# Performance work log

Measured on AMD Instinct MI355X. Metric: run time of the kernel, lower is better.

Reference implementation:

```python
import jax, jax.numpy as jnp
import numpy as np

TEMPERATURE = 0.5


def setup_inputs() -> dict:
    key = jax.random.key(0)
    k1, k2 = jax.random.split(key)
    B, C, H, W = 64, 256, 32, 32
    inputs = jax.random.normal(k1, (B, C, H, W), dtype=jnp.float32)
    targets = jax.random.normal(k2, (B, C, H, W), dtype=jnp.float32)
    return {"inputs": inputs, "targets": targets}


def reference(inputs, targets):
    # [B, C, H, W] -> [H, W, B, C]
    x = jnp.transpose(inputs, (2, 3, 0, 1))
    y = jnp.transpose(targets, (2, 3, 0, 1))
    B = x.shape[-2]
    feats = jnp.concatenate([x, y], axis=-2)  # [H, W, 2B, C]
    eps = jnp.finfo(feats.dtype).eps
    # cosine similarity: normalize each vector with eps-clamped norm, then dot
    norms = jnp.maximum(jnp.linalg.norm(feats, axis=-1, keepdims=True), eps)
    fn = feats / norms
    sim = jnp.einsum('hwic,hwjc->hwij', fn, fn)  # [H, W, 2B, 2B]
    # mask self-similarity diagonal with -inf
    mask = jnp.eye(2 * B, dtype=bool)
    sim = jnp.where(mask, -jnp.inf, sim)
    log_sm = jax.nn.log_softmax(sim / TEMPERATURE, axis=-1)
    pos = jnp.concatenate(
        [jnp.diagonal(log_sm, offset=B, axis1=-2, axis2=-1),
         jnp.diagonal(log_sm, offset=-B, axis1=-2, axis2=-1)],
        axis=-1,
    )  # [H, W, 2B]
    return -jnp.mean(pos)
```

## Files before the change

kernel.cpp:

```cpp
#include <hip/hip_runtime.h>
#include <stdint.h>

#define HWPOS 1024
#define CCH   256
#define RROWS 128
#define EPSF  1.1920928955078125e-07f

typedef __attribute__((ext_vector_type(4))) float float4v;

__device__ __forceinline__ uint32_t pk4_fp8(float a, float b, float c, float d) {
  int v = 0;
  v = __builtin_amdgcn_cvt_pk_fp8_f32(a, b, v, false);
  v = __builtin_amdgcn_cvt_pk_fp8_f32(c, d, v, true);
  return (uint32_t)v;
}


__global__ __launch_bounds__(256, 4) void k_transpose(const float* __restrict__ inp,
                                                      const float* __restrict__ tgt,
                                                      unsigned char* __restrict__ wsF,
                                                      float* __restrict__ out) {
  const int t    = threadIdx.x;
  const int hq   = t & 7;
  const int dd   = (t >> 3) & 15;
  const int rsel = t >> 7;
  const int r    = blockIdx.y * 2 + rsel;
  const int hw0  = blockIdx.x * 32;
  if (blockIdx.x == 0 && blockIdx.y == 0 && t == 0) out[0] = 0.0f;
  const int m = r & 15;
  const int s = dd ^ m;
  const float* src = (r < 64) ? (inp + (size_t)r * CCH * HWPOS)
                              : (tgt + (size_t)(r - 64) * CCH * HWPOS);
  const float* p = src + (size_t)(dd * 16) * HWPOS + hw0 + hq * 4;
  float4 v[16];
#pragma unroll
  for (int e = 0; e < 16; ++e) v[e] = *(const float4*)(p + (size_t)e * HWPOS);
#pragma unroll
  for (int q = 0; q < 4; ++q) {
    float x[16];
#pragma unroll
    for (int e = 0; e < 16; ++e)
      x[e] = (q == 0) ? v[e].x : (q == 1) ? v[e].y : (q == 2) ? v[e].z : v[e].w;
    uint4 o;
    o.x = pk4_fp8(x[0],  x[1],  x[2],  x[3]);
    o.y = pk4_fp8(x[4],  x[5],  x[6],  x[7]);
    o.z = pk4_fp8(x[8],  x[9],  x[10], x[11]);
    o.w = pk4_fp8(x[12], x[13], x[14], x[15]);
    const size_t a = (size_t)(hw0 + hq * 4 + q) * 32768 + (size_t)r * 256 + s * 16;
    *(uint4*)(wsF + a) = o;
  }
}

__global__ __launch_bounds__(512, 4) void k_gram(const unsigned char* __restrict__ wsF,
                                                 float* __restrict__ out) {
  __shared__ unsigned char Fs[32768];
  __shared__ float sInv[RROWS];
  __shared__ float wred[8];
  const int t  = threadIdx.x;
  const int hw = blockIdx.x;
  const int lane = t & 63;
  const int w    = t >> 6;
  const int lid  = lane & 15;
  const int quad = lane >> 4;
  float4v acc[8];
#pragma unroll
  for (int ni = 0; ni < 8; ++ni) acc[ni] = (float4v){0.f, 0.f, 0.f, 0.f};
  const unsigned char* gsrc = wsF + (size_t)hw * 32768;
#pragma unroll
  for (int it = 0; it < 4; ++it) {
    const size_t ch = (size_t)it * 512 + t;
    __builtin_amdgcn_global_load_lds(
        (const __attribute__((address_space(1))) unsigned int*)(gsrc + ch * 16),
        (__attribute__((address_space(3))) unsigned int*)(Fs + ch * 16),
        16, 0, 0);
  }
  __syncthreads();
  const int rowA = (w << 4) | lid;
#pragma unroll
  for (int ks = 0; ks < 8; ++ks) {
    const int d    = 2 * ks + (quad >> 1);
    const int off  = ((d ^ lid) << 4) + (quad & 1) * 8;
    long a = *(const long*)&Fs[rowA * 256 + off];
#pragma unroll
    for (int ni = 0; ni < 8; ++ni) {
      long b = *(const long*)&Fs[(((ni << 4) | lid)) * 256 + off];
      acc[ni] = __builtin_amdgcn_mfma_f32_16x16x32_fp8_fp8(a, b, acc[ni], 0, 0, 0);
    }
  }
  {
    float diagv = 0.f;
#pragma unroll
    for (int ni = 0; ni < 8; ++ni) {
      if (ni == w) {
#pragma unroll
        for (int e = 0; e < 4; ++e)
          if (e == (lid & 3)) diagv = acc[ni][e];
      }
    }
    if ((lid >> 2) == quad) {
      sInv[(w << 4) | lid] = 1.0f / fmaxf(sqrtf(diagv), EPSF);
    }
  }
  __syncthreads();
  float invj[8];
#pragma unroll
  for (int ni = 0; ni < 8; ++ni) invj[ni] = sInv[(ni << 4) | lid];
  const int tj = (w + 4) & 7;
  float lacc = 0.f;
#pragma unroll
  for (int reg = 0; reg < 4; ++reg) {
    const int rloc = quad * 4 + reg;
    const int rg   = (w << 4) | rloc;
    const float invi = sInv[rg];
    float v[8];
#pragma unroll
    for (int ni = 0; ni < 8; ++ni) v[ni] = 2.0f * acc[ni][reg] * invi * invj[ni];
#pragma unroll
    for (int ni = 0; ni < 8; ++ni)
      if (ni == w && lid == rloc) v[ni] = -3.0e38f;
    float mx = v[0];
#pragma unroll
    for (int ni = 1; ni < 8; ++ni) mx = fmaxf(mx, v[ni]);
#pragma unroll
    for (int sh = 1; sh < 16; sh <<= 1) mx = fmaxf(mx, __shfl_xor(mx, sh, 16));
    float sm = 0.f;
#pragma unroll
    for (int ni = 0; ni < 8; ++ni) sm += __expf(v[ni] - mx);
#pragma unroll
    for (int sh = 1; sh < 16; sh <<= 1) sm += __shfl_xor(sm, sh, 16);
    const float lse = mx + __logf(sm);
    float cand = 0.f;
#pragma unroll
    for (int ni = 0; ni < 8; ++ni)
      if (ni == tj) cand = v[ni];
    const float vp = __shfl(cand, rloc, 16);
    lacc += vp - lse;
  }
#pragma unroll
  for (int sh = 1; sh < 64; sh <<= 1) lacc += __shfl_xor(lacc, sh, 64);
  if (lane == 0) wred[w] = lacc;
  __syncthreads();
  if (t == 0) {
    float tot = 0.f;
#pragma unroll
    for (int i = 0; i < 8; ++i) tot += wred[i];
    atomicAdd(out, -tot * (1.0f / 2097152.0f));
  }
}

extern "C" void kernel_launch(void* const* d_in, const int* in_sizes, int n_in,
                              void* d_out, int out_size, void* d_ws, size_t ws_size,
                              hipStream_t stream) {
  const float* inp = (const float*)d_in[0];
  const float* tgt = (const float*)d_in[1];
  unsigned char* wsF = (unsigned char*)d_ws;
  k_transpose<<<dim3(32, 64), 256, 0, stream>>>(inp, tgt, wsF, (float*)d_out);
  k_gram<<<dim3(HWPOS), 512, 0, stream>>>(wsF, (float*)d_out);
}
```

Measured before the change: 174.6 us.

## Stage fp8 transpose through LDS to coalesce workspace writes

The transpose kernel now packs fp8 values into a swizzled shared-memory tile and then writes 128-byte contiguous runs per row to the workspace. Previously each thread stored isolated 16-byte chunks scattered at a 32 KB stride. The block/grid mapping changes to cover 128 hw positions and half of the channels per block, and the XOR swizzle layout expected by the gram kernel is preserved. This adds a barrier and LDS traffic in exchange for better write coalescing.

```diff
diff --git a/kernel.cpp b/kernel.cpp
--- a/kernel.cpp
+++ b/kernel.cpp
@@ -20,21 +20,22 @@
                                                       const float* __restrict__ tgt,
                                                       unsigned char* __restrict__ wsF,
                                                       float* __restrict__ out) {
+  __shared__ uint4 Ls[1024];
   const int t    = threadIdx.x;
-  const int hq   = t & 7;
-  const int dd   = (t >> 3) & 15;
-  const int rsel = t >> 7;
-  const int r    = blockIdx.y * 2 + rsel;
-  const int hw0  = blockIdx.x * 32;
-  if (blockIdx.x == 0 && blockIdx.y == 0 && t == 0) out[0] = 0.0f;
-  const int m = r & 15;
-  const int s = dd ^ m;
+  const int hq   = t & 31;
+  const int ddl  = t >> 5;
+  const int bx   = blockIdx.x;
+  const int r    = blockIdx.y;
+  const int half = blockIdx.z;
+  if (bx == 0 && r == 0 && half == 0 && t == 0) out[0] = 0.0f;
+  const int dd = half * 8 + ddl;
   const float* src = (r < 64) ? (inp + (size_t)r * CCH * HWPOS)
                               : (tgt + (size_t)(r - 64) * CCH * HWPOS);
-  const float* p = src + (size_t)(dd * 16) * HWPOS + hw0 + hq * 4;
+  const float* p = src + (size_t)(dd * 16) * HWPOS + bx * 128 + hq * 4;
   float4 v[16];
 #pragma unroll
   for (int e = 0; e < 16; ++e) v[e] = *(const float4*)(p + (size_t)e * HWPOS);
+  const int sbase = ddl ^ (hq & 7);
 #pragma unroll
   for (int q = 0; q < 4; ++q) {
     float x[16];
@@ -46,8 +47,21 @@
     o.y = pk4_fp8(x[4],  x[5],  x[6],  x[7]);
     o.z = pk4_fp8(x[8],  x[9],  x[10], x[11]);
     o.w = pk4_fp8(x[12], x[13], x[14], x[15]);
-    const size_t a = (size_t)(hw0 + hq * 4 + q) * 32768 + (size_t)r * 256 + s * 16;
-    *(uint4*)(wsF + a) = o;
+    Ls[(hq * 4 + q) * 8 + sbase] = o;
+  }
+  __syncthreads();
+  const int sl = t & 7;
+  const int hb = t >> 3;
+  const int mh = r & 7;
+  const int half_out = half ^ ((r >> 3) & 1);
+  const int ddn = sl ^ mh;
+  const size_t gbase = (size_t)(bx * 128) * 32768 + (size_t)r * 256
+                     + (size_t)(half_out * 128 + sl * 16);
+#pragma unroll
+  for (int j = 0; j < 4; ++j) {
+    const int hwl = hb + 32 * j;
+    uint4 d = Ls[hwl * 8 + (ddn ^ ((hwl >> 2) & 7))];
+    *(uint4*)(wsF + gbase + (size_t)hwl * 32768) = d;
   }
 }
 
@@ -154,6 +168,6 @@
   const float* inp = (const float*)d_in[0];
   const float* tgt = (const float*)d_in[1];
   unsigned char* wsF = (unsigned char*)d_ws;
-  k_transpose<<<dim3(32, 64), 256, 0, stream>>>(inp, tgt, wsF, (float*)d_out);
+  k_transpose<<<dim3(8, 128, 2), 256, 0, stream>>>(inp, tgt, wsF, (float*)d_out);
   k_gram<<<dim3(HWPOS), 512, 0, stream>>>(wsF, (float*)d_out);
 }
```

Result: no change. 177.1 us (+1.4%).
